# Optimization experiments

Hardware: AMD Instinct MI355X
Metric: run time of the kernel (lower is better)

The kernel has to match this reference:

```python
import jax, jax.numpy as jnp
import numpy as np

IMG_H = IMG_W = 14
HEADS = 8
HEAD_DIM = 32
INNER = HEADS * HEAD_DIM  # 256
IN_CH = 384
OUT_CH = 768
HIDDEN = 4 * IN_CH  # 1536
SCALE = HEAD_DIM ** -0.5
EPS = 1e-5


def _relative_index(h, w):
    # static numpy computation, identical to the torch buffer
    yy, xx = np.meshgrid(np.arange(h), np.arange(w), indexing='ij')
    coords = np.stack([yy.ravel(), xx.ravel()])            # [2, N]
    rel = coords[:, :, None] - coords[:, None, :]          # [2, N, N]
    rel[0] += h - 1
    rel[1] += w - 1
    rel[0] *= 2 * w - 1
    return (rel[0] + rel[1]).reshape(-1)                   # [N*N]


def _maxpool3s2p1(x):
    # torch MaxPool2d(3, 2, 1): pad with -inf
    return jax.lax.reduce_window(
        x, -jnp.inf, jax.lax.max,
        window_dimensions=(1, 1, 3, 3),
        window_strides=(1, 1, 2, 2),
        padding=((0, 0), (0, 0), (1, 1), (1, 1)))


def _layernorm(x, g, b):
    mu = jnp.mean(x, axis=-1, keepdims=True)
    var = jnp.mean(jnp.square(x - mu), axis=-1, keepdims=True)
    return (x - mu) * jax.lax.rsqrt(var + EPS) * g + b


def setup_inputs() -> dict:
    key = jax.random.key(0)
    ks = jax.random.split(key, 12)
    s = 0.02
    return {
        'x': jax.random.normal(ks[0], (64, IN_CH, 28, 28), jnp.float32),
        'W_qkv': jax.random.normal(ks[1], (IN_CH, 3 * INNER), jnp.float32) * s,
        'bias_table': jax.random.normal(ks[2], ((2 * IMG_H - 1) * (2 * IMG_W - 1), HEADS), jnp.float32) * s,
        'W_out': jax.random.normal(ks[3], (INNER, OUT_CH), jnp.float32) * s,
        'b_out': jnp.zeros((OUT_CH,), jnp.float32),
        'ln1_g': jnp.ones((IN_CH,), jnp.float32),
        'ln1_b': jnp.zeros((IN_CH,), jnp.float32),
        'ln2_g': jnp.ones((OUT_CH,), jnp.float32),
        'ln2_b': jnp.zeros((OUT_CH,), jnp.float32),
        'W_fc1': jax.random.normal(ks[4], (OUT_CH, HIDDEN), jnp.float32) * s,
        'b_fc1': jnp.zeros((HIDDEN,), jnp.float32),
        'W_fc2': jax.random.normal(ks[5], (HIDDEN, OUT_CH), jnp.float32) * s,
        'b_fc2': jnp.zeros((OUT_CH,), jnp.float32),
        'W_proj': jax.random.normal(ks[6], (OUT_CH, IN_CH), jnp.float32) * s,
    }


def reference(x, W_qkv, bias_table, W_out, b_out, ln1_g, ln1_b, ln2_g, ln2_b,
              W_fc1, b_fc1, W_fc2, b_fc2, W_proj):
    B = x.shape[0]
    N = IMG_H * IMG_W
    rel_idx = jnp.asarray(_relative_index(IMG_H, IMG_W))   # [N*N]

    # --- downsample branch ---
    xp = _maxpool3s2p1(x)                                  # [B, Cin, 14, 14]
    proj = jnp.einsum('bchw,oc->bohw', xp, W_proj)         # 1x1 conv, no bias

    # --- attention branch ---
    xa = _maxpool3s2p1(x)                                  # [B, Cin, 14, 14]
    tokens = xa.reshape(B, IN_CH, N).transpose(0, 2, 1)    # [B, N, Cin]
    tokens = _layernorm(tokens, ln1_g, ln1_b)
    qkv = tokens @ W_qkv                                   # [B, N, 3*INNER]
    q, k, v = jnp.split(qkv, 3, axis=-1)
    def heads(t):
        return t.reshape(B, N, HEADS, HEAD_DIM).transpose(0, 2, 1, 3)  # [B,H,N,D]
    q, k, v = heads(q), heads(k), heads(v)
    dots = jnp.einsum('bhid,bhjd->bhij', q, k) * SCALE     # [B,H,N,N]
    bias = bias_table[rel_idx].reshape(N, N, HEADS).transpose(2, 0, 1)  # [H,N,N]
    attn = jax.nn.softmax(dots + bias[None], axis=-1)
    out = jnp.einsum('bhij,bhjd->bhid', attn, v)           # [B,H,N,D]
    out = out.transpose(0, 2, 1, 3).reshape(B, N, INNER)
    out = out @ W_out + b_out                              # [B, N, Cout]
    attn_map = out.transpose(0, 2, 1).reshape(B, OUT_CH, IMG_H, IMG_W)

    h = proj + attn_map                                    # [B, Cout, 14, 14]

    # --- feed-forward branch ---
    t = h.reshape(B, OUT_CH, N).transpose(0, 2, 1)         # [B, N, Cout]
    t = _layernorm(t, ln2_g, ln2_b)
    t = jax.nn.gelu(t @ W_fc1 + b_fc1, approximate=False)
    t = t @ W_fc2 + b_fc2
    ffn = t.transpose(0, 2, 1).reshape(B, OUT_CH, IMG_H, IMG_W)

    return h + ffn
```

## Files before the change

kernel.cpp:

```cpp
#include <hip/hip_runtime.h>
#include <hip/hip_bf16.h>
#include <cmath>

typedef unsigned short ushortT;
typedef unsigned int u32;
typedef __attribute__((ext_vector_type(8))) short short8;
typedef __attribute__((ext_vector_type(4))) float floatx4;

#define IMG 14
#define NTOK 196
#define BATCH 64
#define M_TOT 12544
#define M_HALF 6272
#define INCH 384
#define OUTCH 768
#define HIDDEN 1536
#define HEADS 8
#define HDIM 32
#define SCALE 0.17677669529663687f

__device__ __forceinline__ float b2f(ushortT u) {
    union { u32 i; float f; } v; v.i = ((u32)u) << 16; return v.f;
}
__device__ __forceinline__ ushortT f2b(float f) {
    union { float f; u32 i; } v; v.f = f;
    u32 r = v.i + 0x7FFFu + ((v.i >> 16) & 1u);
    return (ushortT)(r >> 16);
}

__device__ __forceinline__ void async_ld16(const void* g, void* l) {
    __builtin_amdgcn_global_load_lds(
        (const __attribute__((address_space(1))) u32*)g,
        (__attribute__((address_space(3))) u32*)l, 16, 0, 0);
}

__global__ __launch_bounds__(256) void prep_pool(
    const float* __restrict__ Wqkv, const float* __restrict__ Wout,
    const float* __restrict__ Wfc1, const float* __restrict__ Wfc2,
    const float* __restrict__ Wproj, const float* __restrict__ x,
    const float* __restrict__ bias_tb,
    ushortT* __restrict__ oQkv, ushortT* __restrict__ oOut,
    ushortT* __restrict__ oFc1, ushortT* __restrict__ oFc2,
    ushortT* __restrict__ oProj, ushortT* __restrict__ pooled,
    float* __restrict__ bias_exp) {
    __shared__ __align__(16) char lds_raw[26880];
    int blk = blockIdx.x;
    int tid = threadIdx.x;
    if (blk >= 4608) {
        int idx4 = (blk - 4608) * 256 + tid;
        int h = idx4 / 10816;
        int rem = idx4 - h * 10816;
        int i = rem / 52;
        int j0 = (rem - i * 52) * 4;
        float v[4];
        #pragma unroll
        for (int u = 0; u < 4; ++u) {
            int j = j0 + u;
            float val = 0.f;
            if (i < 196 && j < 196) {
                int iy = i / 14, ix = i - iy * 14;
                int jy = j / 14, jx = j - jy * 14;
                val = bias_tb[((iy - jy + 13) * 27 + (ix - jx + 13)) * 8 + h];
            }
            v[u] = val;
        }
        *(float4*)(bias_exp + (size_t)idx4 * 4) = *(const float4*)v;
        return;
    }
    if (blk >= 3072) {
        int pblk = blk - 3072;
        int cg = pblk % 24, b = pblk / 24;
        float* hm = (float*)lds_raw;
        const float* xsrc = x + ((size_t)b * INCH + cg * 16) * 784;
        for (int t = tid; t < 448; t += 256) {
            int c = t / 28, hrow = t - c * 28;
            const float* rp = xsrc + c * 784 + hrow * 28;
            float r[28];
            #pragma unroll
            for (int u = 0; u < 7; ++u)
                *(float4*)(r + u * 4) = *(const float4*)(rp + u * 4);
            float* hr = hm + (size_t)t * 15;
            #pragma unroll
            for (int j = 0; j < 14; ++j) {
                float a = j ? r[2 * j - 1] : r[0];
                hr[j] = fmaxf(fmaxf(a, r[2 * j]), r[2 * j + 1]);
            }
        }
        __syncthreads();
        for (int chunk = tid; chunk < NTOK * 2; chunk += 256) {
            int n = chunk >> 1, q = chunk & 1;
            int hh = n / IMG, ww = n - hh * IMG;
            int ya = hh ? 2 * hh - 1 : 0;
            int y1 = 2 * hh, y2 = 2 * hh + 1;
            ushortT o[8];
            #pragma unroll
            for (int cc = 0; cc < 8; ++cc) {
                const float* base = hm + (size_t)(q * 8 + cc) * 28 * 15 + ww;
                float mv = fmaxf(fmaxf(base[ya * 15], base[y1 * 15]), base[y2 * 15]);
                o[cc] = f2b(mv);
            }
            *(uint4*)(pooled + ((size_t)b * NTOK + n) * INCH + cg * 16 + q * 8) =
                *(const uint4*)o;
        }
        return;
    }
    if (blk >= 2784) {
        int i = ((blk - 2784) * 256 + tid) * 4;
        float4 v = *(const float4*)(Wproj + i);
        ushortT o[4] = { f2b(v.x), f2b(v.y), f2b(v.z), f2b(v.w) };
        *(uint2*)(oProj + i) = *(const uint2*)o;
        return;
    }
    const float* in; ushortT* out; int R, C, tile;
    if (blk < 288)       { in = Wqkv; out = oQkv; R = 384;  C = 768;  tile = blk; }
    else if (blk < 480)  { in = Wout; out = oOut; R = 256;  C = 768;  tile = blk - 288; }
    else if (blk < 1632) { in = Wfc1; out = oFc1; R = 768;  C = 1536; tile = blk - 480; }
    else                 { in = Wfc2; out = oFc2; R = 1536; C = 768;  tile = blk - 1632; }
    int tilesX = C >> 5;
    int bx = (tile % tilesX) * 32, by = (tile / tilesX) * 32;
    ushortT (*t)[33] = (ushortT (*)[33])lds_raw;
    int tx = tid & 31, ty = tid >> 5;
    #pragma unroll
    for (int i = 0; i < 4; ++i) {
        int r = by + ty * 4 + i;
        t[ty * 4 + i][tx] = f2b(in[(size_t)r * C + bx + tx]);
    }
    __syncthreads();
    #pragma unroll
    for (int i = 0; i < 4; ++i) {
        int r = bx + ty * 4 + i;
        out[(size_t)r * R + by + tx] = t[tx][ty * 4 + i];
    }
}

template <int VE>
__global__ __launch_bounds__(256) void ln_kernel(const ushortT* __restrict__ in,
                                                 const float* __restrict__ gw,
                                                 const float* __restrict__ bw,
                                                 ushortT* __restrict__ out) {
    constexpr int C = 192 * VE;
    int wave = threadIdx.x >> 6, lane = threadIdx.x & 63;
    int m = blockIdx.x * 4 + wave;
    const ushortT* row = in + (size_t)m * C;
    float v[3][VE];
    float s = 0.f, q = 0.f;
    #pragma unroll
    for (int seg = 0; seg < 3; ++seg) {
        int idx = seg * 64 * VE + lane * VE;
        ushortT tmp[VE];
        if constexpr (VE == 2) *(u32*)tmp = *(const u32*)(row + idx);
        else                   *(uint2*)tmp = *(const uint2*)(row + idx);
        #pragma unroll
        for (int k = 0; k < VE; ++k) {
            float f = b2f(tmp[k]);
            v[seg][k] = f;
            s += f;
            q += f * f;
        }
    }
    #pragma unroll
    for (int off = 32; off > 0; off >>= 1) {
        s += __shfl_xor(s, off, 64);
        q += __shfl_xor(q, off, 64);
    }
    float mu = s / (float)C;
    float var = q / (float)C - mu * mu;
    float rs = rsqrtf(var + 1e-5f);
    #pragma unroll
    for (int seg = 0; seg < 3; ++seg) {
        int idx = seg * 64 * VE + lane * VE;
        float g[VE], bb[VE];
        if constexpr (VE == 2) {
            *(float2*)g = *(const float2*)(gw + idx);
            *(float2*)bb = *(const float2*)(bw + idx);
        } else {
            *(float4*)g = *(const float4*)(gw + idx);
            *(float4*)bb = *(const float4*)(bw + idx);
        }
        ushortT o[VE];
        #pragma unroll
        for (int k = 0; k < VE; ++k)
            o[k] = f2b((v[seg][k] - mu) * rs * g[k] + bb[k]);
        if constexpr (VE == 2) *(u32*)(out + (size_t)m * C + idx) = *(const u32*)o;
        else                   *(uint2*)(out + (size_t)m * C + idx) = *(const uint2*)o;
    }
}

__global__ __launch_bounds__(256) void attn_kernel(const ushortT* __restrict__ qkv,
                                                   const float* __restrict__ bias_exp,
                                                   ushortT* __restrict__ attn_out) {
    int bh = blockIdx.x;
    int b = bh >> 3, h = bh & 7;
    __shared__ ushortT Vts[32 * 232];
    __shared__ ushortT Ps[4][16 * 232];
    const int tid = threadIdx.x, wave = tid >> 6, lane = tid & 63;

    const ushortT* qg = qkv + (size_t)bh * 6272;
    const ushortT* kg = qkv + (size_t)(512 + bh) * 6272;
    const uint4* v4 = (const uint4*)(qkv + (size_t)(1024 + bh) * 6272);
    for (int t = tid; t < 784; t += 256) {
        int j = t >> 2, d0 = (t & 3) * 8;
        uint4 v = v4[t];
        const ushortT* vs = (const ushortT*)&v;
        #pragma unroll
        for (int u = 0; u < 8; ++u)
            Vts[(d0 + u) * 232 + j] = vs[u];
    }
    for (int t = tid; t < 1152; t += 256) {
        int d = t / 36, j = 196 + t - d * 36;
        Vts[d * 232 + j] = 0;
    }
    for (int t = tid; t < 1536; t += 256) {
        int w = t / 384, rem = t - w * 384;
        int row = rem / 24, j = 208 + rem - (rem / 24) * 24;
        Ps[w][row * 232 + j] = 0;
    }
    __syncthreads();

    const int fr = (lane & 15), fk = (lane >> 4) * 8;
    short8 kf[13];
    #pragma unroll
    for (int nt = 0; nt < 13; ++nt)
        kf[nt] = *(const short8*)(kg + (nt * 16 + fr) * 32 + fk);

    const int i0r = (lane >> 4) * 4;
    const int colL = lane & 15;
    ushortT* Pw = &Ps[wave][0];

    for (int mt = wave; mt < 13; mt += 4) {
        short8 af = *(const short8*)(qg + (mt * 16 + fr) * 32 + fk);
        floatx4 sc[13];
        #pragma unroll
        for (int nt = 0; nt < 13; ++nt)
            sc[nt] = __builtin_amdgcn_mfma_f32_16x16x32_bf16(
                af, kf[nt], (floatx4){0.f, 0.f, 0.f, 0.f}, 0, 0, 0);

        float rsum[4] = {0.f, 0.f, 0.f, 0.f};
        const float* bb = bias_exp + ((size_t)h * 208 + mt * 16 + i0r) * 208 + colL;
        #pragma unroll
        for (int nt = 0; nt < 13; ++nt) {
            #pragma unroll
            for (int r = 0; r < 4; ++r) {
                float bias = bb[r * 208 + nt * 16];
                float p = __expf(sc[nt][r] * SCALE + bias);
                if (nt == 12 && colL >= 4) p = 0.f;
                rsum[r] += p;
                Pw[(i0r + r) * 232 + nt * 16 + colL] = f2b(p);
            }
        }
        #pragma unroll
        for (int off = 1; off < 16; off <<= 1) {
            #pragma unroll
            for (int r = 0; r < 4; ++r) rsum[r] += __shfl_xor(rsum[r], off, 64);
        }

        floatx4 o[2];
        o[0] = (floatx4){0.f, 0.f, 0.f, 0.f};
        o[1] = (floatx4){0.f, 0.f, 0.f, 0.f};
        #pragma unroll
        for (int kt = 0; kt < 7; ++kt) {
            short8 pf = *(const short8*)(Pw + fr * 232 + kt * 32 + fk);
            #pragma unroll
            for (int n2 = 0; n2 < 2; ++n2) {
                short8 vf = *(const short8*)(Vts + (n2 * 16 + fr) * 232 + kt * 32 + fk);
                o[n2] = __builtin_amdgcn_mfma_f32_16x16x32_bf16(pf, vf, o[n2], 0, 0, 0);
            }
        }
        float invl[4];
        #pragma unroll
        for (int r = 0; r < 4; ++r) invl[r] = 1.f / rsum[r];
        #pragma unroll
        for (int n2 = 0; n2 < 2; ++n2) {
            #pragma unroll
            for (int r = 0; r < 4; ++r) {
                int i = mt * 16 + i0r + r;
                if (i < 196)
                    attn_out[((size_t)(b * 196 + i)) * 256 + h * 32 + n2 * 16 + colL] =
                        f2b(o[n2][r] * invl[r]);
            }
        }
    }
}

template <int BM>
__device__ __forceinline__ void gemm_core(
    const ushortT* __restrict__ A, const ushortT* __restrict__ B,
    int nsteps, int lda, int ldb, int tm, int tn,
    ushortT* As, ushortT* Bs, floatx4 (&acc)[BM / 32][4],
    int tid, int wave, int lane) {
    constexpr int MT = BM / 32;
    constexpr int ATILE = BM * 32;
    const int fr = lane & 15, fk = (lane >> 4) * 8;
    const int wr = (wave >> 1) * (BM / 2), wc = (wave & 1) * 64;
    auto stage = [&](int buf, int k0) {
        const ushortT* Ag = A + (size_t)(tm * BM) * lda + k0;
        const ushortT* Bg = B + (size_t)(tn * 128) * ldb + k0;
        ushortT* Al = As + buf * ATILE;
        ushortT* Bl = Bs + buf * 4096;
        #pragma unroll
        for (int i = 0; i < BM / 64; ++i) {
            int c = tid + i * 256;
            async_ld16(Ag + (size_t)(c >> 2) * lda + (c & 3) * 8, Al + c * 8);
        }
        #pragma unroll
        for (int i = 0; i < 2; ++i) {
            int c = tid + i * 256;
            async_ld16(Bg + (size_t)(c >> 2) * ldb + (c & 3) * 8, Bl + c * 8);
        }
    };
    stage(0, 0);
    for (int t = 0; t < nsteps; ++t) {
        __syncthreads();
        if (t + 1 < nsteps) stage((t + 1) & 1, (t + 1) * 32);
        const ushortT* Ab = As + (t & 1) * ATILE;
        const ushortT* Bb = Bs + (t & 1) * 4096;
        short8 af[MT], bf[4];
        #pragma unroll
        for (int mt = 0; mt < MT; ++mt)
            af[mt] = *(const short8*)(Ab + (wr + mt * 16 + fr) * 32 + fk);
        #pragma unroll
        for (int nt = 0; nt < 4; ++nt)
            bf[nt] = *(const short8*)(Bb + (wc + nt * 16 + fr) * 32 + fk);
        #pragma unroll
        for (int mt = 0; mt < MT; ++mt)
            #pragma unroll
            for (int nt = 0; nt < 4; ++nt)
                acc[mt][nt] = __builtin_amdgcn_mfma_f32_16x16x32_bf16(
                    af[mt], bf[nt], acc[mt][nt], 0, 0, 0);
    }
}

__global__ __launch_bounds__(256) void gemm_qkvproj(
    const ushortT* __restrict__ tln1, const ushortT* __restrict__ wTqkv,
    const ushortT* __restrict__ pooled, const ushortT* __restrict__ wProjB,
    const float* __restrict__ b_out, ushortT* __restrict__ qkvb,
    float* __restrict__ outT) {
    __shared__ ushortT As[2 * 4096];
    __shared__ ushortT Bs[2 * 4096];
    const int tid = threadIdx.x, wave = tid >> 6, lane = tid & 63;
    const int tm = blockIdx.x;
    const int y = blockIdx.y;
    const bool isP = y >= 6;
    const int tn = isP ? y - 6 : y;
    const ushortT* A = isP ? pooled : tln1;
    const ushortT* B = isP ? wProjB : wTqkv;

    floatx4 acc[4][4];
    #pragma unroll
    for (int a = 0; a < 4; ++a)
        #pragma unroll
        for (int c = 0; c < 4; ++c)
            acc[a][c] = (floatx4){0.f, 0.f, 0.f, 0.f};

    gemm_core<128>(A, B, 12, 384, 384, tm, tn, As, Bs, acc, tid, wave, lane);

    const int wr = (wave >> 1) * 64, wc = (wave & 1) * 64;
    const int nb = tn * 128 + wc + (lane & 15);
    const int mbl = wr + ((lane >> 4) << 2);
    if (!isP) {
        #pragma unroll
        for (int nt = 0; nt < 4; ++nt) {
            int n = nb + nt * 16;
            int reg = n >> 8, head = (n >> 5) & 7, d = n & 31;
            #pragma unroll
            for (int mt = 0; mt < 4; ++mt) {
                #pragma unroll
                for (int r = 0; r < 4; ++r) {
                    int m = tm * 128 + mbl + mt * 16 + r;
                    int bb = m / 196, tok = m - bb * 196;
                    qkvb[((size_t)((reg * 512 + bb * 8 + head) * 196 + tok)) * 32 + d] =
                        f2b(acc[mt][nt][r]);
                }
            }
        }
    } else {
        #pragma unroll
        for (int nt = 0; nt < 4; ++nt) {
            int n = nb + nt * 16;
            float bv = b_out[n];
            #pragma unroll
            for (int mt = 0; mt < 4; ++mt) {
                int m0 = tm * 128 + mbl + mt * 16;
                int bb = m0 / 196, tok = m0 - bb * 196;
                float vv[4];
                #pragma unroll
                for (int r = 0; r < 4; ++r) vv[r] = acc[mt][nt][r] + bv;
                *(float4*)(outT + ((size_t)(bb * 768 + n)) * 196 + tok) =
                    *(const float4*)vv;
            }
        }
    }
}

template <int EPI, int BM>
__global__ __launch_bounds__(256) void gemm128p(
    const ushortT* __restrict__ A, const ushortT* __restrict__ B, int K,
    const float* __restrict__ bias, ushortT* __restrict__ outb,
    float* __restrict__ outT, int m_off) {
    __shared__ ushortT As[2 * BM * 32];
    __shared__ ushortT Bs[2 * 4096];
    const int tid = threadIdx.x, wave = tid >> 6, lane = tid & 63;
    const int tm = blockIdx.x, tn = blockIdx.y;
    constexpr int MT = BM / 32;

    floatx4 acc[MT][4];
    #pragma unroll
    for (int a = 0; a < MT; ++a)
        #pragma unroll
        for (int c = 0; c < 4; ++c)
            acc[a][c] = (floatx4){0.f, 0.f, 0.f, 0.f};

    gemm_core<BM>(A, B, K >> 5, K, K, tm, tn, As, Bs, acc, tid, wave, lane);

    const int wr = (wave >> 1) * (BM / 2), wc = (wave & 1) * 64;
    const int nb = tn * 128 + wc + (lane & 15);
    const int mbl = wr + ((lane >> 4) << 2);
    #pragma unroll
    for (int nt = 0; nt < 4; ++nt) {
        int n = nb + nt * 16;
        float bv = (EPI == 2 || EPI == 3) ? bias[n] : 0.f;
        #pragma unroll
        for (int mt = 0; mt < MT; ++mt) {
            int m0 = tm * BM + mbl + mt * 16;
            if constexpr (EPI == 1) {
                int bb = m0 / 196, tok = m0 - bb * 196;
                float* p = outT + ((size_t)(bb * 768 + n)) * 196 + tok;
                float hv[4];
                *(float4*)hv = *(const float4*)p;
                float vv[4];
                #pragma unroll
                for (int r = 0; r < 4; ++r) vv[r] = acc[mt][nt][r] + hv[r];
                *(float4*)p = *(const float4*)vv;
                #pragma unroll
                for (int r = 0; r < 4; ++r)
                    outb[(size_t)(m0 + r) * 768 + n] = f2b(vv[r]);
            } else if constexpr (EPI == 2) {
                #pragma unroll
                for (int r = 0; r < 4; ++r) {
                    float v = acc[mt][nt][r] + bv;
                    float gl = 0.5f * v * (1.f + erff(v * 0.70710678118654752f));
                    outb[(size_t)(m0 + r) * 1536 + n] = f2b(gl);
                }
            } else {
                int mg = m0 + m_off;
                int bb = mg / 196, tok = mg - bb * 196;
                float* p = outT + ((size_t)(bb * 768 + n)) * 196 + tok;
                float hv[4];
                *(float4*)hv = *(const float4*)p;
                float vv[4];
                #pragma unroll
                for (int r = 0; r < 4; ++r) vv[r] = acc[mt][nt][r] + bv + hv[r];
                *(float4*)p = *(const float4*)vv;
            }
        }
    }
}

extern "C" void kernel_launch(void* const* d_in, const int* in_sizes, int n_in,
                              void* d_out, int out_size, void* d_ws, size_t ws_size,
                              hipStream_t stream) {
    const float* x       = (const float*)d_in[0];
    const float* W_qkv   = (const float*)d_in[1];
    const float* bias_tb = (const float*)d_in[2];
    const float* W_out   = (const float*)d_in[3];
    const float* b_out   = (const float*)d_in[4];
    const float* ln1_g   = (const float*)d_in[5];
    const float* ln1_b   = (const float*)d_in[6];
    const float* ln2_g   = (const float*)d_in[7];
    const float* ln2_b   = (const float*)d_in[8];
    const float* W_fc1   = (const float*)d_in[9];
    const float* b_fc1   = (const float*)d_in[10];
    const float* W_fc2   = (const float*)d_in[11];
    const float* b_fc2   = (const float*)d_in[12];
    const float* W_proj  = (const float*)d_in[13];
    float* out = (float*)d_out;

    char* ws = (char*)d_ws;
    ushortT* pooled = (ushortT*)(ws);
    ushortT* tln1   = (ushortT*)(ws + 9633792);
    ushortT* attno  = tln1;
    ushortT* qkvb   = (ushortT*)(ws + 19267584);
    ushortT* tln2   = qkvb;
    ushortT* mid    = (ushortT*)(ws);
    ushortT* htok   = (ushortT*)(ws + 38535168);
    float*   bias_exp = (float*)(ws + 38535168);
    ushortT* wTqkv  = (ushortT*)(ws + 57802752);
    ushortT* wTout  = wTqkv + 768 * 384;
    ushortT* wTfc1  = wTout + 768 * 256;
    ushortT* wTfc2  = wTfc1 + 1536 * 768;
    ushortT* wProjB = wTfc2 + 768 * 1536;
    const size_t weights_end = 57802752 +
        (size_t)(768 * 384 + 768 * 256 + 1536 * 768 + 768 * 1536 + 768 * 384) * 2;
    const bool ffn_full = ws_size >= weights_end + (size_t)M_TOT * HIDDEN * 2;
    ushortT* midf = (ushortT*)(ws + weights_end);

    prep_pool<<<4946, 256, 0, stream>>>(W_qkv, W_out, W_fc1, W_fc2, W_proj, x, bias_tb,
                                        wTqkv, wTout, wTfc1, wTfc2, wProjB, pooled,
                                        bias_exp);

    ln_kernel<2><<<M_TOT / 4, 256, 0, stream>>>(pooled, ln1_g, ln1_b, tln1);

    gemm_qkvproj<<<dim3(98, 12), 256, 0, stream>>>(tln1, wTqkv, pooled, wProjB,
                                                   b_out, qkvb, out);
    attn_kernel<<<512, 256, 0, stream>>>(qkvb, bias_exp, attno);

    gemm128p<1, 64><<<dim3(196, 6), 256, 0, stream>>>(attno, wTout, 256,
                                                      nullptr, htok, out, 0);
    ln_kernel<4><<<M_TOT / 4, 256, 0, stream>>>(htok, ln2_g, ln2_b, tln2);

    if (ffn_full) {
        gemm128p<2, 128><<<dim3(98, 12), 256, 0, stream>>>(tln2, wTfc1, 768,
                                                           b_fc1, midf, nullptr, 0);
        gemm128p<3, 64><<<dim3(196, 6), 256, 0, stream>>>(midf, wTfc2, 1536,
                                                          b_fc2, nullptr, out, 0);
    } else {
        for (int half = 0; half < 2; ++half) {
            const ushortT* a2 = tln2 + (size_t)half * M_HALF * 768;
            gemm128p<2, 128><<<dim3(49, 12), 256, 0, stream>>>(a2, wTfc1, 768,
                                                               b_fc1, mid, nullptr, 0);
            gemm128p<3, 64><<<dim3(98, 6), 256, 0, stream>>>(mid, wTfc2, 1536,
                                                             b_fc2, nullptr, out,
                                                             half * M_HALF);
        }
    }
    (void)in_sizes; (void)n_in; (void)out_size; (void)ws_size;
}
```

Before: 408.1 us.

## Use 8-wave triple-buffered BK=64 GEMM for FFN and 128-row W_out tiles

Replaces the generic gemm128p with a 512-thread gemm8p for the FC1 and FC2 GEMMs. It uses 128x128 tiles with a K-step of 64, triple-buffered async LDS staging, XOR-swizzled shared layout, split A/B prefetch across half-steps, and setprio around the MFMAs. The W_out GEMM moves to a dedicated kernel with 128-row tiles, which halves its grid. The goal is better latency hiding and MFMA utilisation in the dominant FFN GEMMs, at the cost of more LDS (96KB), which limits occupancy.

```diff
diff --git a/kernel.cpp b/kernel.cpp
--- a/kernel.cpp
+++ b/kernel.cpp
@@ -392,49 +392,131 @@
     }
 }
 
-template <int EPI, int BM>
-__global__ __launch_bounds__(256) void gemm128p(
+__global__ __launch_bounds__(256) void gemm_wout(
+    const ushortT* __restrict__ A, const ushortT* __restrict__ B, int K,
+    ushortT* __restrict__ outb, float* __restrict__ outT) {
+    __shared__ ushortT As[2 * 4096];
+    __shared__ ushortT Bs[2 * 4096];
+    const int tid = threadIdx.x, wave = tid >> 6, lane = tid & 63;
+    const int tm = blockIdx.x, tn = blockIdx.y;
+
+    floatx4 acc[4][4];
+    #pragma unroll
+    for (int a = 0; a < 4; ++a)
+        #pragma unroll
+        for (int c = 0; c < 4; ++c)
+            acc[a][c] = (floatx4){0.f, 0.f, 0.f, 0.f};
+
+    gemm_core<128>(A, B, K >> 5, K, K, tm, tn, As, Bs, acc, tid, wave, lane);
+
+    const int wr = (wave >> 1) * 64, wc = (wave & 1) * 64;
+    const int nb = tn * 128 + wc + (lane & 15);
+    const int mbl = wr + ((lane >> 4) << 2);
+    #pragma unroll
+    for (int nt = 0; nt < 4; ++nt) {
+        int n = nb + nt * 16;
+        #pragma unroll
+        for (int mt = 0; mt < 4; ++mt) {
+            int m0 = tm * 128 + mbl + mt * 16;
+            int bb = m0 / 196, tok = m0 - bb * 196;
+            float* p = outT + ((size_t)(bb * 768 + n)) * 196 + tok;
+            float hv[4];
+            *(float4*)hv = *(const float4*)p;
+            float vv[4];
+            #pragma unroll
+            for (int r = 0; r < 4; ++r) vv[r] = acc[mt][nt][r] + hv[r];
+            *(float4*)p = *(const float4*)vv;
+            #pragma unroll
+            for (int r = 0; r < 4; ++r)
+                outb[(size_t)(m0 + r) * 768 + n] = f2b(vv[r]);
+        }
+    }
+}
+
+template <int EPI>
+__global__ __launch_bounds__(512) void gemm8p(
     const ushortT* __restrict__ A, const ushortT* __restrict__ B, int K,
     const float* __restrict__ bias, ushortT* __restrict__ outb,
     float* __restrict__ outT, int m_off) {
-    __shared__ ushortT As[2 * BM * 32];
-    __shared__ ushortT Bs[2 * 4096];
+    __shared__ ushortT As[3][128 * 64];
+    __shared__ ushortT Bs[3][128 * 64];
     const int tid = threadIdx.x, wave = tid >> 6, lane = tid & 63;
     const int tm = blockIdx.x, tn = blockIdx.y;
-    constexpr int MT = BM / 32;
-
-    floatx4 acc[MT][4];
-    #pragma unroll
-    for (int a = 0; a < MT; ++a)
+    const int fr = lane & 15, fk = (lane >> 4) * 8;
+    const int wr = (wave >> 1) * 32, wc = (wave & 1) * 64;
+
+    const int srow = wave * 8 + (lane >> 3);
+    const int scol = ((lane & 7) ^ (lane >> 3)) << 3;
+    const int ldst = wave * 512 + lane * 8;
+    const ushortT* gA = A + (size_t)(tm * 128 + srow) * K + scol;
+    const ushortT* gB = B + (size_t)(tn * 128 + srow) * K + scol;
+
+    auto stageA = [&](int buf, int k0) {
+        async_ld16(gA + k0, &As[buf][ldst]);
+        async_ld16(gA + (size_t)64 * K + k0, &As[buf][ldst + 4096]);
+    };
+    auto stageB = [&](int buf, int k0) {
+        async_ld16(gB + k0, &Bs[buf][ldst]);
+        async_ld16(gB + (size_t)64 * K + k0, &Bs[buf][ldst + 4096]);
+    };
+
+    floatx4 acc[2][4];
+    #pragma unroll
+    for (int a = 0; a < 2; ++a)
         #pragma unroll
         for (int c = 0; c < 4; ++c)
             acc[a][c] = (floatx4){0.f, 0.f, 0.f, 0.f};
 
-    gemm_core<BM>(A, B, K >> 5, K, K, tm, tn, As, Bs, acc, tid, wave, lane);
-
-    const int wr = (wave >> 1) * (BM / 2), wc = (wave & 1) * 64;
-    const int nb = tn * 128 + wc + (lane & 15);
+    const int nsteps = K >> 6;
+    stageA(0, 0); stageB(0, 0);
+    stageA(1, 64); stageB(1, 64);
+    for (int t = 0; t < nsteps; ++t) {
+        const ushortT* Ab = As[t % 3];
+        const ushortT* Bb = Bs[t % 3];
+        #pragma unroll
+        for (int p = 0; p < 2; ++p) {
+            if (p == 0) {
+                if (t + 1 < nsteps) asm volatile("s_waitcnt vmcnt(4)" ::: "memory");
+                else                asm volatile("s_waitcnt vmcnt(0)" ::: "memory");
+            }
+            __builtin_amdgcn_s_barrier();
+            __builtin_amdgcn_sched_barrier(0);
+            if (t + 2 < nsteps) {
+                if (p == 0) stageA((t + 2) % 3, (t + 2) * 64);
+                else        stageB((t + 2) % 3, (t + 2) * 64);
+            }
+            short8 af[2], bf[4];
+            #pragma unroll
+            for (int mt = 0; mt < 2; ++mt) {
+                int r = wr + mt * 16 + fr;
+                af[mt] = *(const short8*)(Ab + r * 64 + ((p * 32 + fk) ^ ((r & 7) << 3)));
+            }
+            #pragma unroll
+            for (int nt = 0; nt < 4; ++nt) {
+                int r = wc + nt * 16 + fr;
+                bf[nt] = *(const short8*)(Bb + r * 64 + ((p * 32 + fk) ^ ((r & 7) << 3)));
+            }
+            __builtin_amdgcn_s_setprio(1);
+            #pragma unroll
+            for (int mt = 0; mt < 2; ++mt)
+                #pragma unroll
+                for (int nt = 0; nt < 4; ++nt)
+                    acc[mt][nt] = __builtin_amdgcn_mfma_f32_16x16x32_bf16(
+                        af[mt], bf[nt], acc[mt][nt], 0, 0, 0);
+            __builtin_amdgcn_s_setprio(0);
+        }
+    }
+
+    const int nb = tn * 128 + wc + fr;
     const int mbl = wr + ((lane >> 4) << 2);
     #pragma unroll
     for (int nt = 0; nt < 4; ++nt) {
         int n = nb + nt * 16;
-        float bv = (EPI == 2 || EPI == 3) ? bias[n] : 0.f;
-        #pragma unroll
-        for (int mt = 0; mt < MT; ++mt) {
-            int m0 = tm * BM + mbl + mt * 16;
-            if constexpr (EPI == 1) {
-                int bb = m0 / 196, tok = m0 - bb * 196;
-                float* p = outT + ((size_t)(bb * 768 + n)) * 196 + tok;
-                float hv[4];
-                *(float4*)hv = *(const float4*)p;
-                float vv[4];
-                #pragma unroll
-                for (int r = 0; r < 4; ++r) vv[r] = acc[mt][nt][r] + hv[r];
-                *(float4*)p = *(const float4*)vv;
-                #pragma unroll
-                for (int r = 0; r < 4; ++r)
-                    outb[(size_t)(m0 + r) * 768 + n] = f2b(vv[r]);
-            } else if constexpr (EPI == 2) {
+        float bv = bias[n];
+        #pragma unroll
+        for (int mt = 0; mt < 2; ++mt) {
+            int m0 = tm * 128 + mbl + mt * 16;
+            if constexpr (EPI == 2) {
                 #pragma unroll
                 for (int r = 0; r < 4; ++r) {
                     float v = acc[mt][nt][r] + bv;
@@ -504,23 +586,22 @@
                                                    b_out, qkvb, out);
     attn_kernel<<<512, 256, 0, stream>>>(qkvb, bias_exp, attno);
 
-    gemm128p<1, 64><<<dim3(196, 6), 256, 0, stream>>>(attno, wTout, 256,
-                                                      nullptr, htok, out, 0);
+    gemm_wout<<<dim3(98, 6), 256, 0, stream>>>(attno, wTout, 256, htok, out);
     ln_kernel<4><<<M_TOT / 4, 256, 0, stream>>>(htok, ln2_g, ln2_b, tln2);
 
     if (ffn_full) {
-        gemm128p<2, 128><<<dim3(98, 12), 256, 0, stream>>>(tln2, wTfc1, 768,
-                                                           b_fc1, midf, nullptr, 0);
-        gemm128p<3, 64><<<dim3(196, 6), 256, 0, stream>>>(midf, wTfc2, 1536,
-                                                          b_fc2, nullptr, out, 0);
+        gemm8p<2><<<dim3(98, 12), 512, 0, stream>>>(tln2, wTfc1, 768,
+                                                    b_fc1, midf, nullptr, 0);
+        gemm8p<3><<<dim3(98, 6), 512, 0, stream>>>(midf, wTfc2, 1536,
+                                                   b_fc2, nullptr, out, 0);
     } else {
         for (int half = 0; half < 2; ++half) {
             const ushortT* a2 = tln2 + (size_t)half * M_HALF * 768;
-            gemm128p<2, 128><<<dim3(49, 12), 256, 0, stream>>>(a2, wTfc1, 768,
-                                                               b_fc1, mid, nullptr, 0);
-            gemm128p<3, 64><<<dim3(98, 6), 256, 0, stream>>>(mid, wTfc2, 1536,
-                                                             b_fc2, nullptr, out,
-                                                             half * M_HALF);
+            gemm8p<2><<<dim3(49, 12), 512, 0, stream>>>(a2, wTfc1, 768,
+                                                        b_fc1, mid, nullptr, 0);
+            gemm8p<3><<<dim3(49, 6), 512, 0, stream>>>(mid, wTfc2, 1536,
+                                                       b_fc2, nullptr, out,
+                                                       half * M_HALF);
         }
     }
     (void)in_sizes; (void)n_in; (void)out_size; (void)ws_size;
```

New measurement: 464.5 us. +13.8%, slower.
